# Kernel optimization log

Hardware: AMD Instinct MI355X
Metric: run time of the kernel (lower is better)

The kernel has to match this reference:

```python
import jax, jax.numpy as jnp
import numpy as np

T, D, H, C = 8, 512, 100, 2  # n_edge_types, dim_in_time+dim_in_node, hidden(=100 in source), predict_class
E, NEG = 100000, 1


def _linear_params(key, fan_in, fan_out, n_types):
    k1, k2 = jax.random.split(key)
    bound = 1.0 / np.sqrt(fan_in)
    W = jax.random.uniform(k1, (n_types, fan_in, fan_out), jnp.float32, -bound, bound)
    b = jax.random.uniform(k2, (n_types, fan_out), jnp.float32, -bound, bound)
    return W, b


def setup_inputs() -> dict:
    key = jax.random.key(0)
    kh, kt, k1, k2, k3 = jax.random.split(key, 5)
    h = jax.random.normal(kh, ((NEG + 2) * E, D), jnp.float32)
    edge_types = jax.random.randint(kt, (E,), 0, T).astype(jnp.int32)
    src_W, src_b = _linear_params(k1, D, H, T)
    dst_W, dst_b = _linear_params(k2, D, H, T)
    out_W, out_b = _linear_params(k3, H, C, T)
    return {"h": h, "src_W": src_W, "src_b": src_b, "dst_W": dst_W,
            "dst_b": dst_b, "out_W": out_W, "out_b": out_b,
            "edge_types": edge_types, "neg_samples": NEG}


def _select_type(all_types, t):
    # all_types: [N, T, F], t: [N] int -> [N, F]
    return jnp.take_along_axis(all_types, t[:, None, None], axis=1)[:, 0]


def reference(h, src_W, src_b, dst_W, dst_b, out_W, out_b, edge_types, neg_samples):
    num_edge = edge_types.shape[0]
    h_src = h[:num_edge]                      # [E, D]
    h_pos_dst = h[num_edge:2 * num_edge]      # [E, D]
    h_neg_dst = h[2 * num_edge:]              # [E*neg, D]
    h_save = h[:2 * num_edge]
    t = edge_types
    t_neg = jnp.repeat(t, neg_samples)        # type of each neg row

    # type-routed linears: compute for all types, then select per-edge type
    src_enc = _select_type(jnp.einsum('ed,tdh->eth', h_src, src_W) + src_b[None], t)          # [E, H]
    pos_enc = _select_type(jnp.einsum('ed,tdh->eth', h_pos_dst, dst_W) + dst_b[None], t)      # [E, H]
    neg_enc = _select_type(jnp.einsum('ed,tdh->eth', h_neg_dst, dst_W) + dst_b[None], t_neg)  # [E*neg, H]

    pos_edge = jax.nn.relu(src_enc + pos_enc)
    neg_edge = jax.nn.relu(jnp.repeat(src_enc, neg_samples, axis=0) + neg_enc)

    pos_out = _select_type(jnp.einsum('eh,thc->etc', pos_edge, out_W) + out_b[None], t)       # [E, C]
    neg_out = _select_type(jnp.einsum('eh,thc->etc', neg_edge, out_W) + out_b[None], t_neg)   # [E*neg, C]

    # source concatenates per-type groups in type order (stable within a type)
    perm = jnp.argsort(t, stable=True)
    pos_pred = pos_out[perm]
    neg_idx = (perm[:, None] * neg_samples + jnp.arange(neg_samples)).reshape(-1)
    neg_pred = neg_out[neg_idx]
    return pos_pred, neg_pred, h_save
```

## Files before the change

### kernel.cpp

```cpp
#include <hip/hip_runtime.h>

constexpr int D_ = 512;
constexpr int H_ = 100;
constexpr int C_ = 2;
constexpr int T_ = 8;

constexpr int TE  = 128;
constexpr int DC  = 32;
constexpr int NC  = D_ / DC;
constexpr int NTH = 256;
constexpr int GRID_MAIN = 256;
constexpr int SB  = 128;
constexpr int STH = 256;

constexpr int WS_CTR  = 26;
constexpr int WS_HIST = 32;
constexpr int WS_SORTED = 32 + SB * T_;

typedef __attribute__((ext_vector_type(8))) short bf16x8;
typedef __attribute__((ext_vector_type(4))) float f32x4;

__device__ __forceinline__ unsigned short bfhi(float x) {
    return (unsigned short)(__builtin_bit_cast(unsigned int, x) >> 16);
}
__device__ __forceinline__ float bfback(unsigned short u) {
    return __builtin_bit_cast(float, (unsigned int)u << 16);
}

__global__ __launch_bounds__(STH) void k_hist(const int* __restrict__ et, int E, int seg,
                                              int* __restrict__ hist) {
    __shared__ int hb[T_];
    const int b = blockIdx.x, tid = threadIdx.x;
    if (tid < T_) hb[tid] = 0;
    __syncthreads();
    const int segLo = b * seg;
    const int segHi = min(E, segLo + seg);
    const int per = (seg + STH - 1) / STH;
    const int lo = segLo + tid * per;
    const int hi = min(segHi, lo + per);
    int c[T_];
#pragma unroll
    for (int j = 0; j < T_; ++j) c[j] = 0;
    for (int i = lo; i < hi; ++i) {
        int ty = et[i];
#pragma unroll
        for (int j = 0; j < T_; ++j) c[j] += (ty == j) ? 1 : 0;
    }
#pragma unroll
    for (int j = 0; j < T_; ++j)
        if (c[j]) atomicAdd(&hb[j], c[j]);
    __syncthreads();
    if (tid < T_) hist[b * T_ + tid] = hb[tid];
}

__global__ __launch_bounds__(SB) void k_scan(int* __restrict__ hist,
                                             int* __restrict__ typeBase,
                                             int* __restrict__ typeCount,
                                             int* __restrict__ tileBase,
                                             int* __restrict__ ctr, int grid0) {
    __shared__ int sc[SB][T_ + 1];
    __shared__ int sbase[T_];
    const int tid = threadIdx.x;
#pragma unroll
    for (int j = 0; j < T_; ++j) sc[tid][j] = hist[tid * T_ + j];
    __syncthreads();
    for (int ofs = 1; ofs < SB; ofs <<= 1) {
        int v[T_];
        if (tid >= ofs) {
#pragma unroll
            for (int j = 0; j < T_; ++j) v[j] = sc[tid - ofs][j];
        }
        __syncthreads();
        if (tid >= ofs) {
#pragma unroll
            for (int j = 0; j < T_; ++j) sc[tid][j] += v[j];
        }
        __syncthreads();
    }
    if (tid == 0) {
        int b = 0, tb = 0;
#pragma unroll
        for (int j = 0; j < T_; ++j) {
            int cntj = sc[SB - 1][j];
            sbase[j] = b;
            typeBase[j] = b;
            typeCount[j] = cntj;
            tileBase[j] = tb;
            b += cntj;
            tb += (cntj + TE - 1) / TE;
        }
        tileBase[T_] = tb;
        ctr[0] = grid0;
    }
    __syncthreads();
#pragma unroll
    for (int j = 0; j < T_; ++j)
        hist[tid * T_ + j] = sbase[j] + (tid ? sc[tid - 1][j] : 0);
}

__global__ __launch_bounds__(STH) void k_scatter(const int* __restrict__ et, int E, int seg,
                                                 const int* __restrict__ blockBase,
                                                 int* __restrict__ sorted_e) {
    __shared__ int sc[STH][T_ + 1];
    const int b = blockIdx.x, tid = threadIdx.x;
    const int segLo = b * seg;
    const int segHi = min(E, segLo + seg);
    const int per = (seg + STH - 1) / STH;
    const int lo = segLo + tid * per;
    const int hi = min(segHi, lo + per);
    int c[T_];
#pragma unroll
    for (int j = 0; j < T_; ++j) c[j] = 0;
    for (int i = lo; i < hi; ++i) {
        int ty = et[i];
#pragma unroll
        for (int j = 0; j < T_; ++j) c[j] += (ty == j) ? 1 : 0;
    }
#pragma unroll
    for (int j = 0; j < T_; ++j) sc[tid][j] = c[j];
    __syncthreads();
    for (int ofs = 1; ofs < STH; ofs <<= 1) {
        int v[T_];
        if (tid >= ofs) {
#pragma unroll
            for (int j = 0; j < T_; ++j) v[j] = sc[tid - ofs][j];
        }
        __syncthreads();
        if (tid >= ofs) {
#pragma unroll
            for (int j = 0; j < T_; ++j) sc[tid][j] += v[j];
        }
        __syncthreads();
    }
    int p[T_];
#pragma unroll
    for (int j = 0; j < T_; ++j)
        p[j] = blockBase[b * T_ + j] + (tid ? sc[tid - 1][j] : 0);
    for (int i = lo; i < hi; ++i) {
        int ty = et[i];
        int r = 0;
#pragma unroll
        for (int j = 0; j < T_; ++j) {
            if (ty == j) { r = p[j]; p[j] = r + 1; }
        }
        sorted_e[r] = i;
    }
}

__device__ __forceinline__ float fold16(float (&v)[16], int ln) {
    float v8[8];
#pragma unroll
    for (int a = 0; a < 8; ++a) {
        float keep = (ln & 1) ? v[2 * a + 1] : v[2 * a];
        float send = (ln & 1) ? v[2 * a] : v[2 * a + 1];
        v8[a] = keep + __shfl_xor(send, 1);
    }
    float v4[4];
#pragma unroll
    for (int a = 0; a < 4; ++a) {
        float keep = (ln & 2) ? v8[2 * a + 1] : v8[2 * a];
        float send = (ln & 2) ? v8[2 * a] : v8[2 * a + 1];
        v4[a] = keep + __shfl_xor(send, 2);
    }
    float v2[2];
#pragma unroll
    for (int a = 0; a < 2; ++a) {
        float keep = (ln & 4) ? v4[2 * a + 1] : v4[2 * a];
        float send = (ln & 4) ? v4[2 * a] : v4[2 * a + 1];
        v2[a] = keep + __shfl_xor(send, 4);
    }
    float keep = (ln & 8) ? v2[1] : v2[0];
    float send = (ln & 8) ? v2[0] : v2[1];
    return keep + __shfl_xor(send, 8);
}

__global__ __launch_bounds__(NTH, 1) void k_main(
    const float* __restrict__ h,
    const float* __restrict__ srcW, const float* __restrict__ srcB,
    const float* __restrict__ dstW, const float* __restrict__ dstB,
    const float* __restrict__ outW, const float* __restrict__ outB,
    const int* __restrict__ sorted_e,
    const int* __restrict__ typeBase, const int* __restrict__ typeCount,
    const int* __restrict__ tileBase,
    int* __restrict__ ctr,
    float* __restrict__ out, int E)
{
    const int tid = threadIdx.x;
    const int w   = tid >> 6;
    const int l   = tid & 63;
    const int ln  = l & 15;
    const int lg  = l >> 4;

    __shared__ __align__(16) float4 stgH[2][3 * TE * (DC / 4)];
    __shared__ __align__(16) unsigned wTu[4 * 4 * 112 * 4];
    __shared__ int eIdx[TE];
    __shared__ int sNext;

    const int nT = tileBase[T_];
    const size_t mStride = (size_t)E * D_;
    float* const outH = out + (size_t)4 * E;

    int cmat[4], clg[4], cn[4], cnld[4], cslot[4];
    bool cok[4];
#pragma unroll
    for (int it = 0; it < 4; ++it) {
        int item = it * 256 + tid;
        cok[it] = item < 896;
        int itc = cok[it] ? item : 0;
        cmat[it] = itc / 448;
        int rem  = itc % 448;
        clg[it]  = rem / 112;
        cn[it]   = rem % 112;
        cnld[it] = (cn[it] < H_) ? cn[it] : (H_ - 1);
        cslot[it] = cn[it] ^ ((cn[it] >> 3) & 7);
    }

    int tile = blockIdx.x;
    while (tile < nT) {
        int t = 0;
#pragma unroll
        for (int j = 1; j < T_; ++j) t += (tile >= tileBase[j]) ? 1 : 0;
        const int i0   = (tile - tileBase[t]) * TE;
        const int cnt  = typeCount[t];
        const int base = typeBase[t];

        if (tid < TE) {
            int p = i0 + tid;
            eIdx[tid] = sorted_e[base + (p < cnt ? p : i0)];
        }
        __syncthreads();

        const int r0 = tid >> 3, s8 = tid & 7;
        const float* rowSrc[4]; float* rowHS[4]; int slotLin[4]; bool gok[4];
#pragma unroll
        for (int rr4 = 0; rr4 < 4; ++rr4) {
            int rr = r0 + rr4 * 32;
            int sw = (rr ^ (rr >> 3)) & 7;
            int c4 = s8 ^ sw;
            int e  = eIdx[rr];
            rowSrc[rr4]  = h    + (size_t)e * D_ + (c4 << 2);
            rowHS[rr4]   = outH + (size_t)e * D_ + (s8 << 2);
            slotLin[rr4] = rr * 8 + c4;
            gok[rr4]     = (i0 + rr) < cnt;
        }

        const float* wsBase = srcW + (size_t)t * D_ * H_;
        const float* wdBase = dstW + (size_t)t * D_ * H_;

        auto stageH = [&](int buf, int d0c) {
            float4* dH = &stgH[buf][0];
#pragma unroll
            for (int m = 0; m < 3; ++m)
#pragma unroll
                for (int rr4 = 0; rr4 < 4; ++rr4)
                    __builtin_amdgcn_global_load_lds(
                        (const __attribute__((address_space(1))) void*)(rowSrc[rr4] + m * mStride + d0c),
                        (__attribute__((address_space(3))) void*)(dH + m * 1024 + rr4 * 256 + tid),
                        16, 0, 0);
        };

        f32x4 acc[6][7];
#pragma unroll
        for (int a = 0; a < 6; ++a)
#pragma unroll
            for (int nt = 0; nt < 7; ++nt) acc[a][nt] = (f32x4){0.f, 0.f, 0.f, 0.f};

        stageH(0, 0);

#pragma unroll 1
        for (int ch = 0; ch < NC; ++ch) {
            const int d0 = ch * DC;
            const int cb = ch & 1;

            __syncthreads();

            float wf[4][8];
#pragma unroll
            for (int it = 0; it < 4; ++it) {
                const float* wb = (cmat[it] ? wdBase : wsBase)
                                + (size_t)(d0 + clg[it] * 8) * H_ + cnld[it];
#pragma unroll
                for (int j = 0; j < 8; ++j) wf[it][j] = wb[(size_t)j * H_];
            }

            if (ch + 1 < NC) stageH(cb ^ 1, d0 + DC);

            const float4* csH = &stgH[cb][0];

#pragma unroll
            for (int m = 0; m < 2; ++m)
#pragma unroll
                for (int rr4 = 0; rr4 < 4; ++rr4) {
                    float4 v = csH[m * 1024 + slotLin[rr4]];
                    if (gok[rr4]) *(float4*)(rowHS[rr4] + m * mStride + d0) = v;
                }

#pragma unroll
            for (int it = 0; it < 4; ++it) {
                if (cok[it]) {
                    unsigned hu[4], lu[4];
#pragma unroll
                    for (int p = 0; p < 4; ++p) {
                        float x0 = wf[it][2 * p], x1 = wf[it][2 * p + 1];
                        unsigned short h0 = bfhi(x0), h1 = bfhi(x1);
                        unsigned short l0 = bfhi(x0 - bfback(h0));
                        unsigned short l1 = bfhi(x1 - bfback(h1));
                        hu[p] = (unsigned)h0 | ((unsigned)h1 << 16);
                        lu[p] = (unsigned)l0 | ((unsigned)l1 << 16);
                    }
                    int bHi = (((cmat[it] * 2 + 0) * 4 + clg[it]) * 112 + cslot[it]) * 4;
                    int bLo = (((cmat[it] * 2 + 1) * 4 + clg[it]) * 112 + cslot[it]) * 4;
                    *(uint4*)&wTu[bHi] = (uint4){hu[0], hu[1], hu[2], hu[3]};
                    *(uint4*)&wTu[bLo] = (uint4){lu[0], lu[1], lu[2], lu[3]};
                }
            }

            asm volatile("s_waitcnt lgkmcnt(0)\n\ts_barrier" ::: "memory");
            __builtin_amdgcn_sched_barrier(0);

            bf16x8 Ahi[6], Alo[6];
#pragma unroll
            for (int a = 0; a < 6; ++a) {
                const int row = (w + 4 * a) * 16 + ln;
                const int swR = (row ^ (row >> 3)) & 7;
                const float4* rp = csH + row * 8;
                float4 x0 = rp[(2 * lg) ^ swR];
                float4 x1 = rp[(2 * lg + 1) ^ swR];
#pragma unroll
                for (int j = 0; j < 4; ++j) {
                    float v0 = ((const float*)&x0)[j];
                    unsigned short hh = bfhi(v0);
                    Ahi[a][j] = (short)hh;
                    Alo[a][j] = (short)bfhi(v0 - bfback(hh));
                }
#pragma unroll
                for (int j = 0; j < 4; ++j) {
                    float v1 = ((const float*)&x1)[j];
                    unsigned short hh = bfhi(v1);
                    Ahi[a][4 + j] = (short)hh;
                    Alo[a][4 + j] = (short)bfhi(v1 - bfback(hh));
                }
            }

#pragma unroll
            for (int nt = 0; nt < 7; ++nt) {
                const int n = nt * 16 + ln;
                const int slotP = n ^ ((n >> 3) & 7);
                bf16x8 B[2][2];
#pragma unroll
                for (int mat = 0; mat < 2; ++mat)
#pragma unroll
                    for (int hl = 0; hl < 2; ++hl)
                        B[mat][hl] = *(const bf16x8*)&wTu[(((mat * 2 + hl) * 4 + lg) * 112 + slotP) * 4];
#pragma unroll
                for (int a = 0; a < 6; ++a) {
                    const int mm = (a < 2) ? 0 : 1;
                    acc[a][nt] = __builtin_amdgcn_mfma_f32_16x16x32_bf16(Ahi[a], B[mm][0], acc[a][nt], 0, 0, 0);
                    acc[a][nt] = __builtin_amdgcn_mfma_f32_16x16x32_bf16(Ahi[a], B[mm][1], acc[a][nt], 0, 0, 0);
                    acc[a][nt] = __builtin_amdgcn_mfma_f32_16x16x32_bf16(Alo[a], B[mm][0], acc[a][nt], 0, 0, 0);
                }
            }
        }

        float sB7[7], dB7[7], woA[7], woB[7];
        bool valn[7];
#pragma unroll
        for (int nt = 0; nt < 7; ++nt) {
            int n = nt * 16 + ln;
            valn[nt] = (n < H_);
            int nc = valn[nt] ? n : (H_ - 1);
            sB7[nt] = srcB[t * H_ + nc];
            dB7[nt] = dstB[t * H_ + nc];
            float2 wo = *(const float2*)(outW + (size_t)t * H_ * C_ + nc * C_);
            woA[nt] = wo.x; woB[nt] = wo.y;
        }

        float pp[16], nn[16];
#pragma unroll
        for (int i = 0; i < 16; ++i) { pp[i] = 0.f; nn[i] = 0.f; }
#pragma unroll
        for (int nt = 0; nt < 7; ++nt)
#pragma unroll
            for (int a = 0; a < 2; ++a)
#pragma unroll
                for (int reg = 0; reg < 4; ++reg) {
                    float sv = acc[a][nt][reg] + sB7[nt] + dB7[nt];
                    float pe = fmaxf(acc[a + 2][nt][reg] + sv, 0.f);
                    float ne = fmaxf(acc[a + 4][nt][reg] + sv, 0.f);
                    pe = valn[nt] ? pe : 0.f;
                    ne = valn[nt] ? ne : 0.f;
                    const int ix = a * 8 + reg * 2;
                    pp[ix]     = fmaf(pe, woA[nt], pp[ix]);
                    pp[ix + 1] = fmaf(pe, woB[nt], pp[ix + 1]);
                    nn[ix]     = fmaf(ne, woA[nt], nn[ix]);
                    nn[ix + 1] = fmaf(ne, woB[nt], nn[ix + 1]);
                }

        float totP = fold16(pp, ln);
        float totN = fold16(nn, ln);
        {
            const int c   = ln & 1;
            const int reg = (ln >> 1) & 3;
            const int aa  = (ln >> 3) & 1;
            const int e   = (w + 4 * aa) * 16 + lg * 4 + reg;
            if (i0 + e < cnt) {
                float ob = outB[t * C_ + c];
                size_t pidx = (size_t)(base + i0 + e) * C_ + c;
                out[pidx] = totP + ob;
                out[(size_t)C_ * E + pidx] = totN + ob;
            }
        }

        __syncthreads();
        if (tid == 0) sNext = atomicAdd(ctr, 1);
        __syncthreads();
        tile = sNext;
    }
}

extern "C" void kernel_launch(void* const* d_in, const int* in_sizes, int n_in,
                              void* d_out, int out_size, void* d_ws, size_t ws_size,
                              hipStream_t stream) {
    (void)n_in; (void)out_size; (void)ws_size;
    const float* h    = (const float*)d_in[0];
    const float* srcW = (const float*)d_in[1];
    const float* srcB = (const float*)d_in[2];
    const float* dstW = (const float*)d_in[3];
    const float* dstB = (const float*)d_in[4];
    const float* outW = (const float*)d_in[5];
    const float* outB = (const float*)d_in[6];
    const int*   et   = (const int*)d_in[7];
    const int E = in_sizes[7];

    float* out = (float*)d_out;
    int* ws = (int*)d_ws;
    int* typeBase  = ws;
    int* typeCount = ws + 8;
    int* tileBase  = ws + 16;
    int* ctr       = ws + WS_CTR;
    int* hist      = ws + WS_HIST;
    int* sorted_e  = ws + WS_SORTED;

    const int seg = (E + SB - 1) / SB;
    k_hist<<<SB, STH, 0, stream>>>(et, E, seg, hist);
    k_scan<<<1, SB, 0, stream>>>(hist, typeBase, typeCount, tileBase, ctr, GRID_MAIN);
    k_scatter<<<SB, STH, 0, stream>>>(et, E, seg, hist, sorted_e);

    k_main<<<GRID_MAIN, NTH, 0, stream>>>(h, srcW, srcB, dstW, dstB, outW, outB,
                                          sorted_e, typeBase, typeCount, tileBase,
                                          ctr, out, E);
}
```

Baseline: 1.050 ms.

## Double block to 512 threads, split IO waves, double-buffer weight tiles

The block grows from 256 to 512 threads, and each wave now owns one 16-row slice across the src, pos and neg matrices, so per-thread accumulators drop from 6x7 to 3x7 fragments. Only the first 256 threads issue the h staging loads, the h_save copy and the weight conversion. The converted weight tile is double-buffered so the next chunk's weights are loaded and converted while MFMAs run on the current one. Launch bounds now request 2 blocks per CU for more latency hiding, at the cost of doubled weight LDS, fewer registers per thread and imbalance between IO and compute waves.

```diff
diff --git a/kernel.cpp b/kernel.cpp
--- a/kernel.cpp
+++ b/kernel.cpp
@@ -8,7 +8,7 @@
 constexpr int TE  = 128;
 constexpr int DC  = 32;
 constexpr int NC  = D_ / DC;
-constexpr int NTH = 256;
+constexpr int NTH = 512;
 constexpr int GRID_MAIN = 256;
 constexpr int SB  = 128;
 constexpr int STH = 256;
@@ -174,7 +174,7 @@
     return keep + __shfl_xor(send, 8);
 }
 
-__global__ __launch_bounds__(NTH, 1) void k_main(
+__global__ __launch_bounds__(NTH, 2) void k_main(
     const float* __restrict__ h,
     const float* __restrict__ srcW, const float* __restrict__ srcB,
     const float* __restrict__ dstW, const float* __restrict__ dstB,
@@ -186,13 +186,14 @@
     float* __restrict__ out, int E)
 {
     const int tid = threadIdx.x;
-    const int w   = tid >> 6;
+    const int w8  = tid >> 6;
     const int l   = tid & 63;
     const int ln  = l & 15;
     const int lg  = l >> 4;
+    const bool isIO = tid < 256;
 
     __shared__ __align__(16) float4 stgH[2][3 * TE * (DC / 4)];
-    __shared__ __align__(16) unsigned wTu[4 * 4 * 112 * 4];
+    __shared__ __align__(16) unsigned wTu[2][4 * 4 * 112 * 4];
     __shared__ int eIdx[TE];
     __shared__ int sNext;
 
@@ -200,20 +201,27 @@
     const size_t mStride = (size_t)E * D_;
     float* const outH = out + (size_t)4 * E;
 
-    int cmat[4], clg[4], cn[4], cnld[4], cslot[4];
+    int cmat[4], clg[4], cnld[4], cslot[4];
     bool cok[4];
-#pragma unroll
-    for (int it = 0; it < 4; ++it) {
-        int item = it * 256 + tid;
-        cok[it] = item < 896;
-        int itc = cok[it] ? item : 0;
-        cmat[it] = itc / 448;
-        int rem  = itc % 448;
-        clg[it]  = rem / 112;
-        cn[it]   = rem % 112;
-        cnld[it] = (cn[it] < H_) ? cn[it] : (H_ - 1);
-        cslot[it] = cn[it] ^ ((cn[it] >> 3) & 7);
-    }
+    if (isIO) {
+#pragma unroll
+        for (int it = 0; it < 4; ++it) {
+            int item = it * 256 + tid;
+            cok[it] = item < 896;
+            int itc = cok[it] ? item : 0;
+            cmat[it] = itc / 448;
+            int rem  = itc % 448;
+            clg[it]  = rem / 112;
+            int cn   = rem % 112;
+            cnld[it] = (cn < H_) ? cn : (H_ - 1);
+            cslot[it] = cn ^ ((cn >> 3) & 7);
+        }
+    }
+
+    const int rA  = w8 * 16 + ln;
+    const int swA = (rA ^ (rA >> 3)) & 7;
+    const int sl0 = (2 * lg) ^ swA;
+    const int sl1 = (2 * lg + 1) ^ swA;
 
     int tile = blockIdx.x;
     while (tile < nT) {
@@ -230,22 +238,24 @@
         }
         __syncthreads();
 
-        const int r0 = tid >> 3, s8 = tid & 7;
-        const float* rowSrc[4]; float* rowHS[4]; int slotLin[4]; bool gok[4];
-#pragma unroll
-        for (int rr4 = 0; rr4 < 4; ++rr4) {
-            int rr = r0 + rr4 * 32;
-            int sw = (rr ^ (rr >> 3)) & 7;
-            int c4 = s8 ^ sw;
-            int e  = eIdx[rr];
-            rowSrc[rr4]  = h    + (size_t)e * D_ + (c4 << 2);
-            rowHS[rr4]   = outH + (size_t)e * D_ + (s8 << 2);
-            slotLin[rr4] = rr * 8 + c4;
-            gok[rr4]     = (i0 + rr) < cnt;
-        }
-
         const float* wsBase = srcW + (size_t)t * D_ * H_;
         const float* wdBase = dstW + (size_t)t * D_ * H_;
+
+        const float* rowSrc[4]; float* rowHS[4]; int slotLin[4]; bool gok[4];
+        if (isIO) {
+            const int r0 = tid >> 3, s8 = tid & 7;
+#pragma unroll
+            for (int rr4 = 0; rr4 < 4; ++rr4) {
+                int rr = r0 + rr4 * 32;
+                int sw = (rr ^ (rr >> 3)) & 7;
+                int c4 = s8 ^ sw;
+                int e  = eIdx[rr];
+                rowSrc[rr4]  = h    + (size_t)e * D_ + (c4 << 2);
+                rowHS[rr4]   = outH + (size_t)e * D_ + (s8 << 2);
+                slotLin[rr4] = rr * 8 + c4;
+                gok[rr4]     = (i0 + rr) < cnt;
+            }
+        }
 
         auto stageH = [&](int buf, int d0c) {
             float4* dH = &stgH[buf][0];
@@ -258,43 +268,16 @@
                         (__attribute__((address_space(3))) void*)(dH + m * 1024 + rr4 * 256 + tid),
                         16, 0, 0);
         };
-
-        f32x4 acc[6][7];
-#pragma unroll
-        for (int a = 0; a < 6; ++a)
-#pragma unroll
-            for (int nt = 0; nt < 7; ++nt) acc[a][nt] = (f32x4){0.f, 0.f, 0.f, 0.f};
-
-        stageH(0, 0);
-
-#pragma unroll 1
-        for (int ch = 0; ch < NC; ++ch) {
-            const int d0 = ch * DC;
-            const int cb = ch & 1;
-
-            __syncthreads();
-
-            float wf[4][8];
+        auto loadW = [&](int d0c, float (&wf)[4][8]) {
 #pragma unroll
             for (int it = 0; it < 4; ++it) {
                 const float* wb = (cmat[it] ? wdBase : wsBase)
-                                + (size_t)(d0 + clg[it] * 8) * H_ + cnld[it];
+                                + (size_t)(d0c + clg[it] * 8) * H_ + cnld[it];
 #pragma unroll
                 for (int j = 0; j < 8; ++j) wf[it][j] = wb[(size_t)j * H_];
             }
-
-            if (ch + 1 < NC) stageH(cb ^ 1, d0 + DC);
-
-            const float4* csH = &stgH[cb][0];
-
-#pragma unroll
-            for (int m = 0; m < 2; ++m)
-#pragma unroll
-                for (int rr4 = 0; rr4 < 4; ++rr4) {
-                    float4 v = csH[m * 1024 + slotLin[rr4]];
-                    if (gok[rr4]) *(float4*)(rowHS[rr4] + m * mStride + d0) = v;
-                }
-
+        };
+        auto convW = [&](int buf, const float (&wf)[4][8]) {
 #pragma unroll
             for (int it = 0; it < 4; ++it) {
                 if (cok[it]) {
@@ -310,35 +293,68 @@
                     }
                     int bHi = (((cmat[it] * 2 + 0) * 4 + clg[it]) * 112 + cslot[it]) * 4;
                     int bLo = (((cmat[it] * 2 + 1) * 4 + clg[it]) * 112 + cslot[it]) * 4;
-                    *(uint4*)&wTu[bHi] = (uint4){hu[0], hu[1], hu[2], hu[3]};
-                    *(uint4*)&wTu[bLo] = (uint4){lu[0], lu[1], lu[2], lu[3]};
+                    *(uint4*)&wTu[buf][bHi] = (uint4){hu[0], hu[1], hu[2], hu[3]};
+                    *(uint4*)&wTu[buf][bLo] = (uint4){lu[0], lu[1], lu[2], lu[3]};
                 }
             }
-
-            asm volatile("s_waitcnt lgkmcnt(0)\n\ts_barrier" ::: "memory");
-            __builtin_amdgcn_sched_barrier(0);
-
-            bf16x8 Ahi[6], Alo[6];
-#pragma unroll
-            for (int a = 0; a < 6; ++a) {
-                const int row = (w + 4 * a) * 16 + ln;
-                const int swR = (row ^ (row >> 3)) & 7;
-                const float4* rp = csH + row * 8;
-                float4 x0 = rp[(2 * lg) ^ swR];
-                float4 x1 = rp[(2 * lg + 1) ^ swR];
+        };
+
+        f32x4 acc[3][7];
+#pragma unroll
+        for (int s = 0; s < 3; ++s)
+#pragma unroll
+            for (int nt = 0; nt < 7; ++nt) acc[s][nt] = (f32x4){0.f, 0.f, 0.f, 0.f};
+
+        if (isIO) {
+            stageH(0, 0);
+            float wf0[4][8];
+            loadW(0, wf0);
+            convW(0, wf0);
+        }
+
+#pragma unroll 1
+        for (int ch = 0; ch < NC; ++ch) {
+            const int d0 = ch * DC;
+            const int cb = ch & 1;
+
+            __syncthreads();
+
+            const float4* csH = &stgH[cb][0];
+
+            if (isIO) {
+                const bool more = (ch + 1) < NC;
+                float wf[4][8];
+                if (more) loadW(d0 + DC, wf);
+                if (more) stageH(cb ^ 1, d0 + DC);
+#pragma unroll
+                for (int m = 0; m < 2; ++m)
+#pragma unroll
+                    for (int rr4 = 0; rr4 < 4; ++rr4) {
+                        float4 v = csH[m * 1024 + slotLin[rr4]];
+                        if (gok[rr4]) *(float4*)(rowHS[rr4] + m * mStride + d0) = v;
+                    }
+                if (more) convW(cb ^ 1, wf);
+            }
+
+            bf16x8 Ahi[3], Alo[3];
+#pragma unroll
+            for (int s = 0; s < 3; ++s) {
+                const float4* rp = csH + s * 1024 + rA * 8;
+                float4 x0 = rp[sl0];
+                float4 x1 = rp[sl1];
 #pragma unroll
                 for (int j = 0; j < 4; ++j) {
                     float v0 = ((const float*)&x0)[j];
                     unsigned short hh = bfhi(v0);
-                    Ahi[a][j] = (short)hh;
-                    Alo[a][j] = (short)bfhi(v0 - bfback(hh));
+                    Ahi[s][j] = (short)hh;
+                    Alo[s][j] = (short)bfhi(v0 - bfback(hh));
                 }
 #pragma unroll
                 for (int j = 0; j < 4; ++j) {
                     float v1 = ((const float*)&x1)[j];
                     unsigned short hh = bfhi(v1);
-                    Ahi[a][4 + j] = (short)hh;
-                    Alo[a][4 + j] = (short)bfhi(v1 - bfback(hh));
+                    Ahi[s][4 + j] = (short)hh;
+                    Alo[s][4 + j] = (short)bfhi(v1 - bfback(hh));
                 }
             }
 
@@ -351,63 +367,58 @@
                 for (int mat = 0; mat < 2; ++mat)
 #pragma unroll
                     for (int hl = 0; hl < 2; ++hl)
-                        B[mat][hl] = *(const bf16x8*)&wTu[(((mat * 2 + hl) * 4 + lg) * 112 + slotP) * 4];
-#pragma unroll
-                for (int a = 0; a < 6; ++a) {
-                    const int mm = (a < 2) ? 0 : 1;
-                    acc[a][nt] = __builtin_amdgcn_mfma_f32_16x16x32_bf16(Ahi[a], B[mm][0], acc[a][nt], 0, 0, 0);
-                    acc[a][nt] = __builtin_amdgcn_mfma_f32_16x16x32_bf16(Ahi[a], B[mm][1], acc[a][nt], 0, 0, 0);
-                    acc[a][nt] = __builtin_amdgcn_mfma_f32_16x16x32_bf16(Alo[a], B[mm][0], acc[a][nt], 0, 0, 0);
+                        B[mat][hl] = *(const bf16x8*)&wTu[cb][(((mat * 2 + hl) * 4 + lg) * 112 + slotP) * 4];
+#pragma unroll
+                for (int s = 0; s < 3; ++s) {
+                    const int mm = (s == 0) ? 0 : 1;
+                    acc[s][nt] = __builtin_amdgcn_mfma_f32_16x16x32_bf16(Ahi[s], B[mm][0], acc[s][nt], 0, 0, 0);
+                    acc[s][nt] = __builtin_amdgcn_mfma_f32_16x16x32_bf16(Ahi[s], B[mm][1], acc[s][nt], 0, 0, 0);
+                    acc[s][nt] = __builtin_amdgcn_mfma_f32_16x16x32_bf16(Alo[s], B[mm][0], acc[s][nt], 0, 0, 0);
                 }
             }
         }
 
-        float sB7[7], dB7[7], woA[7], woB[7];
-        bool valn[7];
-#pragma unroll
-        for (int nt = 0; nt < 7; ++nt) {
-            int n = nt * 16 + ln;
-            valn[nt] = (n < H_);
-            int nc = valn[nt] ? n : (H_ - 1);
-            sB7[nt] = srcB[t * H_ + nc];
-            dB7[nt] = dstB[t * H_ + nc];
-            float2 wo = *(const float2*)(outW + (size_t)t * H_ * C_ + nc * C_);
-            woA[nt] = wo.x; woB[nt] = wo.y;
-        }
-
-        float pp[16], nn[16];
-#pragma unroll
-        for (int i = 0; i < 16; ++i) { pp[i] = 0.f; nn[i] = 0.f; }
-#pragma unroll
-        for (int nt = 0; nt < 7; ++nt)
-#pragma unroll
-            for (int a = 0; a < 2; ++a)
+        {
+            float sB7[7], dB7[7], woA[7], woB[7];
+            bool valn[7];
+#pragma unroll
+            for (int nt = 0; nt < 7; ++nt) {
+                int n = nt * 16 + ln;
+                valn[nt] = (n < H_);
+                int nc = valn[nt] ? n : (H_ - 1);
+                sB7[nt] = srcB[t * H_ + nc];
+                dB7[nt] = dstB[t * H_ + nc];
+                float2 wo = *(const float2*)(outW + (size_t)t * H_ * C_ + nc * C_);
+                woA[nt] = wo.x; woB[nt] = wo.y;
+            }
+
+            float v16[16];
+#pragma unroll
+            for (int i = 0; i < 16; ++i) v16[i] = 0.f;
+#pragma unroll
+            for (int nt = 0; nt < 7; ++nt)
 #pragma unroll
                 for (int reg = 0; reg < 4; ++reg) {
-                    float sv = acc[a][nt][reg] + sB7[nt] + dB7[nt];
-                    float pe = fmaxf(acc[a + 2][nt][reg] + sv, 0.f);
-                    float ne = fmaxf(acc[a + 4][nt][reg] + sv, 0.f);
+                    float sv = acc[0][nt][reg] + sB7[nt] + dB7[nt];
+                    float pe = fmaxf(acc[1][nt][reg] + sv, 0.f);
+                    float ne = fmaxf(acc[2][nt][reg] + sv, 0.f);
                     pe = valn[nt] ? pe : 0.f;
                     ne = valn[nt] ? ne : 0.f;
-                    const int ix = a * 8 + reg * 2;
-                    pp[ix]     = fmaf(pe, woA[nt], pp[ix]);
-                    pp[ix + 1] = fmaf(pe, woB[nt], pp[ix + 1]);
-                    nn[ix]     = fmaf(ne, woA[nt], nn[ix]);
-                    nn[ix + 1] = fmaf(ne, woB[nt], nn[ix + 1]);
+                    v16[reg * 2 + 0]     = fmaf(pe, woA[nt], v16[reg * 2 + 0]);
+                    v16[reg * 2 + 1]     = fmaf(pe, woB[nt], v16[reg * 2 + 1]);
+                    v16[8 + reg * 2 + 0] = fmaf(ne, woA[nt], v16[8 + reg * 2 + 0]);
+                    v16[8 + reg * 2 + 1] = fmaf(ne, woB[nt], v16[8 + reg * 2 + 1]);
                 }
 
-        float totP = fold16(pp, ln);
-        float totN = fold16(nn, ln);
-        {
+            float tot = fold16(v16, ln);
             const int c   = ln & 1;
             const int reg = (ln >> 1) & 3;
-            const int aa  = (ln >> 3) & 1;
-            const int e   = (w + 4 * aa) * 16 + lg * 4 + reg;
+            const int pn  = ln >> 3;
+            const int e   = w8 * 16 + lg * 4 + reg;
             if (i0 + e < cnt) {
-                float ob = outB[t * C_ + c];
+                float val = tot + outB[t * C_ + c];
                 size_t pidx = (size_t)(base + i0 + e) * C_ + c;
-                out[pidx] = totP + ob;
-                out[(size_t)C_ * E + pidx] = totN + ob;
+                out[(pn ? (size_t)C_ * E : (size_t)0) + pidx] = val;
             }
         }
 
```

Result: slower. 1.173 ms (+11.7%).

## Precompute split-bf16 weight tiles in a prepass and stream them via async LDS loads

Applied to the files above, without the earlier changes.

Adds a prepass kernel that converts the per-type src/dst weights into hi/lo bf16 pairs, already swizzled in the LDS layout, and writes them to a workspace buffer. The main kernel then double-buffers these tiles into shared memory with global_load_lds alongside the h staging. This removes the per-chunk strided scalar weight loads, the conversion ALU work and one barrier from the inner loop. The cost is an extra kernel launch, extra LDS for two weight buffers, and more global traffic per chunk, since the precomputed hi/lo data is larger than the raw fp32 weights.

```diff
diff --git a/kernel.cpp b/kernel.cpp
--- a/kernel.cpp
+++ b/kernel.cpp
@@ -16,6 +16,7 @@
 constexpr int WS_CTR  = 26;
 constexpr int WS_HIST = 32;
 constexpr int WS_SORTED = 32 + SB * T_;
+constexpr int WS_WPRE = 131072;
 
 typedef __attribute__((ext_vector_type(8))) short bf16x8;
 typedef __attribute__((ext_vector_type(4))) float f32x4;
@@ -147,6 +148,45 @@
     }
 }
 
+__global__ __launch_bounds__(256) void k_prew(const float* __restrict__ srcW,
+                                              const float* __restrict__ dstW,
+                                              unsigned* __restrict__ wPre) {
+    const int flat = blockIdx.x * 256 + threadIdx.x;
+    const int n    = flat % 112;
+    int rest = flat / 112;
+    const int lgm = rest % 8;
+    const int mat = lgm >> 2, lg = lgm & 3;
+    rest /= 8;
+    const int ch = rest % 16, t = rest / 16;
+
+    float x[8];
+    if (n < H_) {
+        const float* W = (mat ? dstW : srcW) + (size_t)t * D_ * H_
+                       + (size_t)(ch * 32 + lg * 8) * H_ + n;
+#pragma unroll
+        for (int j = 0; j < 8; ++j) x[j] = W[(size_t)j * H_];
+    } else {
+#pragma unroll
+        for (int j = 0; j < 8; ++j) x[j] = 0.f;
+    }
+    unsigned hu[4], lu[4];
+#pragma unroll
+    for (int p = 0; p < 4; ++p) {
+        float x0 = x[2 * p], x1 = x[2 * p + 1];
+        unsigned short h0 = bfhi(x0), h1 = bfhi(x1);
+        unsigned short l0 = bfhi(x0 - bfback(h0));
+        unsigned short l1 = bfhi(x1 - bfback(h1));
+        hu[p] = (unsigned)h0 | ((unsigned)h1 << 16);
+        lu[p] = (unsigned)l0 | ((unsigned)l1 << 16);
+    }
+    const int slot = n ^ ((n >> 3) & 7);
+    const unsigned bse = (unsigned)(t * 16 + ch) * 7168u;
+    unsigned hiA = bse + (unsigned)(((mat * 2 + 0) * 4 + lg) * 448 + slot * 4);
+    unsigned loA = bse + (unsigned)(((mat * 2 + 1) * 4 + lg) * 448 + slot * 4);
+    *(uint4*)&wPre[hiA] = (uint4){hu[0], hu[1], hu[2], hu[3]};
+    *(uint4*)&wPre[loA] = (uint4){lu[0], lu[1], lu[2], lu[3]};
+}
+
 __device__ __forceinline__ float fold16(float (&v)[16], int ln) {
     float v8[8];
 #pragma unroll
@@ -176,12 +216,12 @@
 
 __global__ __launch_bounds__(NTH, 1) void k_main(
     const float* __restrict__ h,
-    const float* __restrict__ srcW, const float* __restrict__ srcB,
-    const float* __restrict__ dstW, const float* __restrict__ dstB,
+    const float* __restrict__ srcB, const float* __restrict__ dstB,
     const float* __restrict__ outW, const float* __restrict__ outB,
     const int* __restrict__ sorted_e,
     const int* __restrict__ typeBase, const int* __restrict__ typeCount,
     const int* __restrict__ tileBase,
+    const unsigned* __restrict__ wPre,
     int* __restrict__ ctr,
     float* __restrict__ out, int E)
 {
@@ -192,28 +232,13 @@
     const int lg  = l >> 4;
 
     __shared__ __align__(16) float4 stgH[2][3 * TE * (DC / 4)];
-    __shared__ __align__(16) unsigned wTu[4 * 4 * 112 * 4];
+    __shared__ __align__(16) unsigned wB[2][7168];
     __shared__ int eIdx[TE];
     __shared__ int sNext;
 
     const int nT = tileBase[T_];
     const size_t mStride = (size_t)E * D_;
     float* const outH = out + (size_t)4 * E;
-
-    int cmat[4], clg[4], cn[4], cnld[4], cslot[4];
-    bool cok[4];
-#pragma unroll
-    for (int it = 0; it < 4; ++it) {
-        int item = it * 256 + tid;
-        cok[it] = item < 896;
-        int itc = cok[it] ? item : 0;
-        cmat[it] = itc / 448;
-        int rem  = itc % 448;
-        clg[it]  = rem / 112;
-        cn[it]   = rem % 112;
-        cnld[it] = (cn[it] < H_) ? cn[it] : (H_ - 1);
-        cslot[it] = cn[it] ^ ((cn[it] >> 3) & 7);
-    }
 
     int tile = blockIdx.x;
     while (tile < nT) {
@@ -244,8 +269,7 @@
             gok[rr4]     = (i0 + rr) < cnt;
         }
 
-        const float* wsBase = srcW + (size_t)t * D_ * H_;
-        const float* wdBase = dstW + (size_t)t * D_ * H_;
+        const float4* const wPreT = (const float4*)(wPre + (size_t)t * 16 * 7168);
 
         auto stageH = [&](int buf, int d0c) {
             float4* dH = &stgH[buf][0];
@@ -258,6 +282,16 @@
                         (__attribute__((address_space(3))) void*)(dH + m * 1024 + rr4 * 256 + tid),
                         16, 0, 0);
         };
+        auto stageW = [&](int buf, int chl) {
+            const float4* src = wPreT + chl * 1792;
+            float4* dst = (float4*)&wB[buf][0];
+#pragma unroll
+            for (int it = 0; it < 7; ++it)
+                __builtin_amdgcn_global_load_lds(
+                    (const __attribute__((address_space(1))) void*)(src + it * 256 + tid),
+                    (__attribute__((address_space(3))) void*)(dst + it * 256 + tid),
+                    16, 0, 0);
+        };
 
         f32x4 acc[6][7];
 #pragma unroll
@@ -266,6 +300,7 @@
             for (int nt = 0; nt < 7; ++nt) acc[a][nt] = (f32x4){0.f, 0.f, 0.f, 0.f};
 
         stageH(0, 0);
+        stageW(0, 0);
 
 #pragma unroll 1
         for (int ch = 0; ch < NC; ++ch) {
@@ -274,16 +309,10 @@
 
             __syncthreads();
 
-            float wf[4][8];
-#pragma unroll
-            for (int it = 0; it < 4; ++it) {
-                const float* wb = (cmat[it] ? wdBase : wsBase)
-                                + (size_t)(d0 + clg[it] * 8) * H_ + cnld[it];
-#pragma unroll
-                for (int j = 0; j < 8; ++j) wf[it][j] = wb[(size_t)j * H_];
+            if (ch + 1 < NC) {
+                stageH(cb ^ 1, d0 + DC);
+                stageW(cb ^ 1, ch + 1);
             }
-
-            if (ch + 1 < NC) stageH(cb ^ 1, d0 + DC);
 
             const float4* csH = &stgH[cb][0];
 
@@ -294,29 +323,6 @@
                     float4 v = csH[m * 1024 + slotLin[rr4]];
                     if (gok[rr4]) *(float4*)(rowHS[rr4] + m * mStride + d0) = v;
                 }
-
-#pragma unroll
-            for (int it = 0; it < 4; ++it) {
-                if (cok[it]) {
-                    unsigned hu[4], lu[4];
-#pragma unroll
-                    for (int p = 0; p < 4; ++p) {
-                        float x0 = wf[it][2 * p], x1 = wf[it][2 * p + 1];
-                        unsigned short h0 = bfhi(x0), h1 = bfhi(x1);
-                        unsigned short l0 = bfhi(x0 - bfback(h0));
-                        unsigned short l1 = bfhi(x1 - bfback(h1));
-                        hu[p] = (unsigned)h0 | ((unsigned)h1 << 16);
-                        lu[p] = (unsigned)l0 | ((unsigned)l1 << 16);
-                    }
-                    int bHi = (((cmat[it] * 2 + 0) * 4 + clg[it]) * 112 + cslot[it]) * 4;
-                    int bLo = (((cmat[it] * 2 + 1) * 4 + clg[it]) * 112 + cslot[it]) * 4;
-                    *(uint4*)&wTu[bHi] = (uint4){hu[0], hu[1], hu[2], hu[3]};
-                    *(uint4*)&wTu[bLo] = (uint4){lu[0], lu[1], lu[2], lu[3]};
-                }
-            }
-
-            asm volatile("s_waitcnt lgkmcnt(0)\n\ts_barrier" ::: "memory");
-            __builtin_amdgcn_sched_barrier(0);
 
             bf16x8 Ahi[6], Alo[6];
 #pragma unroll
@@ -351,7 +357,7 @@
                 for (int mat = 0; mat < 2; ++mat)
 #pragma unroll
                     for (int hl = 0; hl < 2; ++hl)
-                        B[mat][hl] = *(const bf16x8*)&wTu[(((mat * 2 + hl) * 4 + lg) * 112 + slotP) * 4];
+                        B[mat][hl] = *(const bf16x8*)&wB[cb][(((mat * 2 + hl) * 4 + lg) * 112 + slotP) * 4];
 #pragma unroll
                 for (int a = 0; a < 6; ++a) {
                     const int mm = (a < 2) ? 0 : 1;
@@ -440,13 +446,15 @@
     int* ctr       = ws + WS_CTR;
     int* hist      = ws + WS_HIST;
     int* sorted_e  = ws + WS_SORTED;
+    unsigned* wPre = (unsigned*)(ws + WS_WPRE);
 
     const int seg = (E + SB - 1) / SB;
     k_hist<<<SB, STH, 0, stream>>>(et, E, seg, hist);
     k_scan<<<1, SB, 0, stream>>>(hist, typeBase, typeCount, tileBase, ctr, GRID_MAIN);
     k_scatter<<<SB, STH, 0, stream>>>(et, E, seg, hist, sorted_e);
-
-    k_main<<<GRID_MAIN, NTH, 0, stream>>>(h, srcW, srcB, dstW, dstB, outW, outB,
+    k_prew<<<448, 256, 0, stream>>>(srcW, dstW, wPre);
+
+    k_main<<<GRID_MAIN, NTH, 0, stream>>>(h, srcB, dstB, outW, outB,
                                           sorted_e, typeBase, typeCount, tileBase,
-                                          ctr, out, E);
-}
+                                          wPre, ctr, out, E);
+}
```

Measured after the change: 1.049 ms. Within noise of the previous version (-0.1%).
